# Kernel optimization log

Hardware: AMD Instinct MI355X
Metric: run time of the kernel (lower is better)

The kernel has to match this reference:

```python
import jax, jax.numpy as jnp
import numpy as np
import math

B, N, C, A, H = 1, 320, 128, 32, 4  # batch, n_res, rep_2d channels, attn channels, heads


def _layernorm(x, w, b, eps=1e-5):
    mu = jnp.mean(x, axis=-1, keepdims=True)
    var = jnp.var(x, axis=-1, keepdims=True)
    return (x - mu) * jax.lax.rsqrt(var + eps) * w + b


def setup_inputs() -> dict:
    key = jax.random.key(0)
    ks = jax.random.split(key, 12)
    s = 0.02
    return {
        "x2d": jax.random.normal(ks[0], (B, N, N, C), dtype=jnp.float32),
        "mask": jnp.ones((B, N, N), dtype=jnp.float32),
        "norm_w": jnp.ones((C,), dtype=jnp.float32),
        "norm_b": jnp.zeros((C,), dtype=jnp.float32),
        "Wq": jax.random.normal(ks[1], (C, A * H), dtype=jnp.float32) * s,
        "Wk": jax.random.normal(ks[2], (C, A * H), dtype=jnp.float32) * s,
        "Wv": jax.random.normal(ks[3], (C, A * H), dtype=jnp.float32) * s,
        "Wb": jax.random.normal(ks[4], (C, H), dtype=jnp.float32) * s,
        "Wg": jax.random.normal(ks[5], (C, A * H), dtype=jnp.float32) * s,
        "bg": jnp.zeros((A * H,), dtype=jnp.float32),
        "Wo": jax.random.normal(ks[6], (A * H, C), dtype=jnp.float32) * s,
        "bo": jnp.zeros((C,), dtype=jnp.float32),
    }


def reference(x2d, mask, norm_w, norm_b, Wq, Wk, Wv, Wb, Wg, bg, Wo, bo):
    xn = _layernorm(x2d, norm_w, norm_b)                      # [B,N,N,C]
    # note: torch .view(..., A, H) splits the output channel as (A, H)
    q = (xn @ Wq).reshape(B, N, N, A, H)
    k = (xn @ Wk).reshape(B, N, N, A, H)
    v = (xn @ Wv).reshape(B, N, N, A, H)
    b = xn @ Wb                                               # [B,N,N,H] -> b[b,j,k,h]
    g = jax.nn.sigmoid((xn @ Wg + bg).reshape(B, N, N, A, H))
    w = jnp.einsum('bijch,bikch->bijkh', q, k) / math.sqrt(A)
    # torch: b.unsqueeze(1).transpose(2,3) => w[b,i,j,k,h] += b[b,k,j,h]
    w = w + jnp.transpose(b, (0, 2, 1, 3))[:, None]           # [B,1,N,N,H]
    w = (w + 100.0) * mask[:, :, None, :, None] - 100.0
    w = jax.nn.softmax(w, axis=-2)                            # over k
    out = jnp.einsum('bijkh,bikch->bijch', w, v) * g          # [B,N,N,A,H]
    out = out.reshape(B, N, N, A * H) @ Wo + bo               # [B,N,N,C]
    out = out * mask[..., None]
    return out
```

## Files before the change

### kernel.cpp

```cpp
#include <hip/hip_runtime.h>
#include <hip/hip_bf16.h>
#include <math.h>

#define N 320
#define C 128
#define A 32
#define H 4
#define NPOS (N*N)

typedef __attribute__((ext_vector_type(8))) __bf16 bf16x8;
typedef __attribute__((ext_vector_type(16))) float f32x16;

union frag_u { int4 i; bf16x8 v; unsigned u[4]; };

#define MFMA32(va, vb, vc) __builtin_amdgcn_mfma_f32_32x32x16_bf16((va), (vb), (vc), 0, 0, 0)

#define WAVE_LDS_FENCE() do { \
    asm volatile("s_waitcnt lgkmcnt(0)" ::: "memory"); \
    __builtin_amdgcn_sched_barrier(0); \
} while (0)

static __device__ __forceinline__ unsigned pk_bf16(float lo, float hi) {
    union { __hip_bfloat162 h; unsigned u; } cv;
    cv.h = __float22bfloat162_rn(make_float2(lo, hi));
    return cv.u;
}

static __device__ __forceinline__ float bf16_to_f32(unsigned short u) {
    union { unsigned u; float f; } c;
    c.u = ((unsigned)u) << 16;
    return c.f;
}

static __device__ __forceinline__ float u32_as_f32(unsigned u) {
    union { unsigned u; float f; } c;
    c.u = u;
    return c.f;
}

__global__ __launch_bounds__(256)
void wprep_kernel(const float* __restrict__ Wq,
                  const float* __restrict__ Wk,
                  const float* __restrict__ Wv,
                  const float* __restrict__ Wg,
                  const float* __restrict__ Wo,
                  unsigned short* __restrict__ WF) {
    const float isq = 0.17677669529663687f;
    int tid = blockIdx.x * 256 + threadIdx.x;
    int lane = tid & 63;
    int kk = (tid >> 6) & 7;
    int ct = (tid >> 9) & 3;
    int mat = tid >> 11;
    const float* src = (mat == 0) ? Wq : (mat == 1) ? Wk : (mat == 2) ? Wv
                     : (mat == 3) ? Wg : Wo;
    float scl = (mat == 0) ? isq : 1.0f;
    int col = ct * 32 + (lane & 31);
    int c0 = kk * 16 + (lane >> 5) * 8;
    float v[8];
    #pragma unroll
    for (int e = 0; e < 8; e++) {
        int rr = c0 + e;
        int srow = (mat == 4) ? (((rr & 31) << 2) | (rr >> 5)) : rr;
        v[e] = src[(size_t)srow * 128 + col] * scl;
    }
    int4 out;
    out.x = pk_bf16(v[0], v[1]);
    out.y = pk_bf16(v[2], v[3]);
    out.z = pk_bf16(v[4], v[5]);
    out.w = pk_bf16(v[6], v[7]);
    *(int4*)((char*)WF + (size_t)tid * 16) = out;
}

__global__ __launch_bounds__(256)
void btrans_kernel(const float* __restrict__ Bp, unsigned short* __restrict__ BpTb) {
    __shared__ float tile[64][65];
    const int b = blockIdx.x;
    const int h = b / 25;
    const int bk = (b % 25) / 5;
    const int bj = b % 5;
    const int k0 = bk * 64, j0 = bj * 64;
    const float* src = Bp + (size_t)h * NPOS;
    unsigned short* dst = BpTb + (size_t)h * NPOS;
    const int t = threadIdx.x;
    #pragma unroll
    for (int u = 0; u < 16; ++u) {
        int idx = u * 256 + t;
        int kk = idx >> 6, jj = idx & 63;
        tile[kk][jj] = src[(size_t)(k0 + kk) * N + j0 + jj];
    }
    __syncthreads();
    #pragma unroll
    for (int u = 0; u < 16; ++u) {
        int idx = u * 256 + t;
        int jj = idx >> 6, kk = idx & 63;
        dst[(size_t)(j0 + jj) * N + k0 + kk] =
            (unsigned short)(pk_bf16(tile[kk][jj], 0.f) & 0xffffu);
    }
}

__global__ __launch_bounds__(256)
void ln_proj_kernel(const float* __restrict__ x2d,
                    const float* __restrict__ norm_w,
                    const float* __restrict__ norm_b,
                    const float* __restrict__ Wb,
                    const float* __restrict__ bg,
                    const unsigned short* __restrict__ WF,
                    unsigned short* __restrict__ Qb,
                    unsigned short* __restrict__ Kb,
                    unsigned short* __restrict__ Vta,
                    unsigned short* __restrict__ Gb,
                    float* __restrict__ Bp) {
    __shared__ __align__(16) unsigned char shbuf[16896];
    unsigned char* xnb = shbuf;

    const int t = threadIdx.x;
    const int gpos0 = blockIdx.x * 32;

    {
        const int r = t >> 3, s = t & 7;
        const float4* src = (const float4*)(x2d + (size_t)(gpos0 + r) * 128 + s * 16);
        float4 xv[4];
        #pragma unroll
        for (int u = 0; u < 4; u++) xv[u] = src[u];
        float sum = 0.f, sq = 0.f;
        #pragma unroll
        for (int u = 0; u < 4; u++) {
            sum += xv[u].x + xv[u].y + xv[u].z + xv[u].w;
            sq += xv[u].x * xv[u].x + xv[u].y * xv[u].y
                + xv[u].z * xv[u].z + xv[u].w * xv[u].w;
        }
        sum += __shfl_xor(sum, 1); sum += __shfl_xor(sum, 2); sum += __shfl_xor(sum, 4);
        sq  += __shfl_xor(sq, 1);  sq  += __shfl_xor(sq, 2);  sq  += __shfl_xor(sq, 4);
        float mean = sum * (1.0f / 128.0f);
        float var  = sq * (1.0f / 128.0f) - mean * mean;
        float rstd = rsqrtf(var + 1e-5f);

        const float4* wsrc = (const float4*)(norm_w + s * 16);
        const float4* bsrc = (const float4*)(norm_b + s * 16);
        const float4* wb4  = (const float4*)Wb;
        float pb0 = 0.f, pb1 = 0.f, pb2 = 0.f, pb3 = 0.f;
        float4 xe;
        #pragma unroll
        for (int u = 0; u < 4; u++) {
            float4 wv = wsrc[u], bv = bsrc[u], x4 = xv[u];
            float4 xn;
            xn.x = (x4.x - mean) * rstd * wv.x + bv.x;
            xn.y = (x4.y - mean) * rstd * wv.y + bv.y;
            xn.z = (x4.z - mean) * rstd * wv.z + bv.z;
            xn.w = (x4.w - mean) * rstd * wv.w + bv.w;
            int cb = s * 16 + u * 4;
            float4 w0 = wb4[cb + 0], w1 = wb4[cb + 1], w2 = wb4[cb + 2], w3 = wb4[cb + 3];
            pb0 = fmaf(xn.x, w0.x, fmaf(xn.y, w1.x, fmaf(xn.z, w2.x, fmaf(xn.w, w3.x, pb0))));
            pb1 = fmaf(xn.x, w0.y, fmaf(xn.y, w1.y, fmaf(xn.z, w2.y, fmaf(xn.w, w3.y, pb1))));
            pb2 = fmaf(xn.x, w0.z, fmaf(xn.y, w1.z, fmaf(xn.z, w2.z, fmaf(xn.w, w3.z, pb2))));
            pb3 = fmaf(xn.x, w0.w, fmaf(xn.y, w1.w, fmaf(xn.z, w2.w, fmaf(xn.w, w3.w, pb3))));
            if (u & 1) {
                int g = s * 2 + (u >> 1);
                int4 gr;
                gr.x = pk_bf16(xe.x, xe.y);
                gr.y = pk_bf16(xe.z, xe.w);
                gr.z = pk_bf16(xn.x, xn.y);
                gr.w = pk_bf16(xn.z, xn.w);
                *(int4*)(xnb + r * 256 + ((g ^ (r & 7)) << 4)) = gr;
            } else {
                xe = xn;
            }
        }
        pb0 += __shfl_xor(pb0, 1); pb0 += __shfl_xor(pb0, 2); pb0 += __shfl_xor(pb0, 4);
        pb1 += __shfl_xor(pb1, 1); pb1 += __shfl_xor(pb1, 2); pb1 += __shfl_xor(pb1, 4);
        pb2 += __shfl_xor(pb2, 1); pb2 += __shfl_xor(pb2, 2); pb2 += __shfl_xor(pb2, 4);
        pb3 += __shfl_xor(pb3, 1); pb3 += __shfl_xor(pb3, 2); pb3 += __shfl_xor(pb3, 4);
        if (s < 4) {
            float pbsel = (s == 0) ? pb0 : (s == 1) ? pb1 : (s == 2) ? pb2 : pb3;
            Bp[(size_t)s * NPOS + gpos0 + r] = pbsel;
        }
    }
    __syncthreads();

    const int lane = t & 63;
    const int w = t >> 6;
    const int col = lane & 31;
    const int hi = lane >> 5;

    frag_u af[8];
    #pragma unroll
    for (int kk = 0; kk < 8; kk++)
        af[kk].i = *(const int4*)(xnb + col * 256 + (((kk * 2 + hi) ^ (col & 7)) << 4));
    __syncthreads();

    const char* wf = (const char*)WF + (size_t)w * 4 * 8 * 1024;
    float* stage_w = (float*)shbuf + w * 1056;

    for (int ct = 0; ct < 4; ct++) {
        f32x16 acc;
        #pragma unroll
        for (int r = 0; r < 16; r++) acc[r] = 0.f;
        #pragma unroll
        for (int kk = 0; kk < 8; kk++) {
            frag_u bf;
            bf.i = *(const int4*)(wf + (ct * 8 + kk) * 1024 + lane * 16);
            acc = MFMA32(af[kk].v, bf.v, acc);
        }
        #pragma unroll
        for (int r = 0; r < 16; r++) {
            int patr = (r & 3) + 8 * (r >> 2) + 4 * hi;
            stage_w[col * 33 + patr] = acc[r];
        }
        WAVE_LDS_FENCE();
        if (w < 2) {
            char* dst = (w == 0) ? (char*)Qb : (char*)Kb;
            #pragma unroll
            for (int h = 0; h < 4; h++) {
                float f[4];
                #pragma unroll
                for (int e = 0; e < 4; e++)
                    f[e] = stage_w[((hi * 4 + e) * 4 + h) * 33 + col];
                uint2 val;
                val.x = pk_bf16(f[0], f[1]);
                val.y = pk_bf16(f[2], f[3]);
                *(uint2*)(dst + ((size_t)(h * 4 + ct) * NPOS + gpos0 + col) * 16 + hi * 8) = val;
            }
        } else if (w == 2) {
            int cc = col, half = hi;
            int plane = (cc & 3) * 32 + ct * 8 + (cc >> 2);
            unsigned pk[8];
            #pragma unroll
            for (int j2 = 0; j2 < 8; j2++)
                pk[j2] = pk_bf16(stage_w[cc * 33 + half * 16 + 2 * j2],
                                 stage_w[cc * 33 + half * 16 + 2 * j2 + 1]);
            int4* dst = (int4*)((char*)Vta + ((size_t)plane * NPOS + gpos0 + half * 16) * 2);
            dst[0] = make_int4(pk[0], pk[1], pk[2], pk[3]);
            dst[1] = make_int4(pk[4], pk[5], pk[6], pk[7]);
        } else {
            #pragma unroll
            for (int h = 0; h < 4; h++) {
                float f[4];
                #pragma unroll
                for (int e = 0; e < 4; e++) {
                    float z = stage_w[((hi * 4 + e) * 4 + h) * 33 + col]
                            + bg[ct * 32 + (hi * 4 + e) * 4 + h];
                    f[e] = 1.0f / (1.0f + __expf(-z));
                }
                uint2 val;
                val.x = pk_bf16(f[0], f[1]);
                val.y = pk_bf16(f[2], f[3]);
                *(uint2*)((char*)Gb + ((size_t)(h * 4 + ct) * NPOS + gpos0 + col) * 16 + hi * 8) = val;
            }
        }
        WAVE_LDS_FENCE();
    }
}

__global__ __launch_bounds__(320, 2)
void attn_kernel(const unsigned short* __restrict__ Qb,
                 const unsigned short* __restrict__ Kb,
                 const unsigned short* __restrict__ Vta,
                 const unsigned short* __restrict__ Gb,
                 const unsigned short* __restrict__ BpTb,
                 const float* __restrict__ mask,
                 unsigned short* __restrict__ Ob) {
    __shared__ __align__(16) unsigned char smem[21120];
    __shared__ float mparr[320];
    __shared__ float m2arr[320];

    const int i = blockIdx.x >> 2;
    const int h = blockIdx.x & 3;
    const int t = threadIdx.x;
    const int lane = t & 63;
    const int w = t >> 6;
    const int col = lane & 31;
    const int hi = lane >> 5;
    const int jt0 = w * 64;

    frag_u qf[2][2];
    const char* qplane = (const char*)Qb + ((size_t)(h * 4) * NPOS + (size_t)i * N) * 16;
    #pragma unroll
    for (int jt = 0; jt < 2; ++jt) {
        int jrow = jt0 + jt * 32 + col;
        #pragma unroll
        for (int cf = 0; cf < 2; ++cf) {
            int g = cf * 2 + hi;
            qf[jt][cf].i = *(const int4*)(qplane + ((size_t)g * NPOS + jrow) * 16);
        }
    }

    const char* kpl = (const char*)Kb + ((size_t)(h * 4) * NPOS + (size_t)i * N) * 16;

    const char* vbsrc = (const char*)Vta + ((size_t)h * 32 * NPOS + (size_t)i * N) * 2;
    #pragma unroll
    for (int it = 0; it < 4; ++it) {
        int tt = t + it * 320;
        int a = tt / 40, kg = tt % 40;
        int4 val = *(const int4*)(vbsrc + (size_t)a * NPOS * 2 + kg * 16);
        *(int4*)(smem + a * 640 + ((kg ^ (a & 7)) << 4)) = val;
    }
    {
        int kt_ = t >> 5, hi_ = (t >> 4) & 1, r_ = t & 15;
        int k = kt_ * 32 + (r_ & 3) + 8 * (r_ >> 2) + 4 * hi_;
        float m_ = mask[(size_t)i * N + k];
        mparr[t] = m_;
        m2arr[t] = fmaf(100.f, m_, -100.f);
    }
    frag_u kf0, kf1, kf0n, kf1n;
    kf0.i = *(const int4*)(kpl + ((size_t)hi * NPOS + col) * 16);
    kf1.i = *(const int4*)(kpl + ((size_t)(2 + hi) * NPOS + col) * 16);
    __syncthreads();

    f32x16 accO[2];
    #pragma unroll
    for (int r = 0; r < 16; ++r) { accO[0][r] = 0.f; accO[1][r] = 0.f; }
    float lsum[2] = { 0.f, 0.f };

    const unsigned short* br0 = BpTb + (size_t)h * NPOS + (size_t)(jt0 + col) * N + 4 * hi;
    const unsigned short* br1 = br0 + (size_t)32 * N;

    uint2 b0[4], b1[4];
    #pragma unroll
    for (int q = 0; q < 4; ++q) b0[q] = *(const uint2*)(br0 + 8 * q);

#define PROCESS_JT(JT, BB)                                                      \
    {                                                                           \
        f32x16 S;                                                               \
        _Pragma("unroll") for (int r = 0; r < 16; ++r) S[r] = 0.f;              \
        __builtin_amdgcn_s_setprio(1);                                          \
        S = MFMA32(kf0.v, qf[JT][0].v, S);                                      \
        S = MFMA32(kf1.v, qf[JT][1].v, S);                                      \
        __builtin_amdgcn_s_setprio(0);                                          \
        float pe[16];                                                           \
        float l0 = 0.f, l1 = 0.f, l2 = 0.f, l3 = 0.f;                           \
        _Pragma("unroll") for (int q = 0; q < 4; ++q) {                         \
            float bb0 = u32_as_f32(BB[q].x << 16);                              \
            float bb1 = u32_as_f32(BB[q].x & 0xffff0000u);                      \
            float bb2 = u32_as_f32(BB[q].y << 16);                              \
            float bb3 = u32_as_f32(BB[q].y & 0xffff0000u);                      \
            float sv0 = fmaf(S[4*q+0] + bb0, mk4[q].x, m2v[q].x);               \
            float sv1 = fmaf(S[4*q+1] + bb1, mk4[q].y, m2v[q].y);               \
            float sv2 = fmaf(S[4*q+2] + bb2, mk4[q].z, m2v[q].z);               \
            float sv3 = fmaf(S[4*q+3] + bb3, mk4[q].w, m2v[q].w);               \
            pe[4*q+0] = __expf(sv0); pe[4*q+1] = __expf(sv1);                   \
            pe[4*q+2] = __expf(sv2); pe[4*q+3] = __expf(sv3);                   \
            l0 += pe[4*q+0]; l1 += pe[4*q+1];                                   \
            l2 += pe[4*q+2]; l3 += pe[4*q+3];                                   \
        }                                                                       \
        lsum[JT] += (l0 + l1) + (l2 + l3);                                      \
        unsigned p[8];                                                          \
        _Pragma("unroll") for (int q = 0; q < 8; ++q)                           \
            p[q] = pk_bf16(pe[2 * q], pe[2 * q + 1]);                           \
        unsigned x0 = p[0], y0 = p[2];                                          \
        unsigned x1 = p[1], y1 = p[3];                                          \
        unsigned x2 = p[4], y2 = p[6];                                          \
        unsigned x3 = p[5], y3 = p[7];                                          \
        asm("v_permlane32_swap_b32 %0, %1" : "+v"(x0), "+v"(y0));               \
        asm("v_permlane32_swap_b32 %0, %1" : "+v"(x1), "+v"(y1));               \
        asm("v_permlane32_swap_b32 %0, %1" : "+v"(x2), "+v"(y2));               \
        asm("v_permlane32_swap_b32 %0, %1" : "+v"(x3), "+v"(y3));               \
        frag_u bf0, bf1;                                                        \
        bf0.u[0] = x0; bf0.u[1] = x1; bf0.u[2] = y0; bf0.u[3] = y1;             \
        bf1.u[0] = x2; bf1.u[1] = x3; bf1.u[2] = y2; bf1.u[3] = y3;             \
        __builtin_amdgcn_s_setprio(1);                                          \
        accO[JT] = MFMA32(vf0.v, bf0.v, accO[JT]);                              \
        accO[JT] = MFMA32(vf1.v, bf1.v, accO[JT]);                              \
        __builtin_amdgcn_s_setprio(0);                                          \
    }

    for (int kt = 0; kt < 10; ++kt) {
        const int kbase = kt * 32;
        frag_u vf0, vf1;
        vf0.i = *(const int4*)(smem + col * 640 + (((kt * 4 + 0 + hi) ^ (col & 7)) << 4));
        vf1.i = *(const int4*)(smem + col * 640 + (((kt * 4 + 2 + hi) ^ (col & 7)) << 4));

        if (kt < 9) {
            int krn = kbase + 32 + col;
            kf0n.i = *(const int4*)(kpl + ((size_t)hi * NPOS + krn) * 16);
            kf1n.i = *(const int4*)(kpl + ((size_t)(2 + hi) * NPOS + krn) * 16);
        }

        float4 mk4[4], m2v[4];
        const float* mp  = mparr + kbase + hi * 16;
        const float* m2p = m2arr + kbase + hi * 16;
        #pragma unroll
        for (int q = 0; q < 4; ++q) {
            mk4[q] = *(const float4*)(mp + 4 * q);
            m2v[q] = *(const float4*)(m2p + 4 * q);
        }

        #pragma unroll
        for (int q = 0; q < 4; ++q) b1[q] = *(const uint2*)(br1 + kbase + 8 * q);

        PROCESS_JT(0, b0)

        if (kt < 9) {
            #pragma unroll
            for (int q = 0; q < 4; ++q) b0[q] = *(const uint2*)(br0 + kbase + 32 + 8 * q);
        }

        PROCESS_JT(1, b1)

        kf0 = kf0n;
        kf1 = kf1n;
    }
#undef PROCESS_JT

    __syncthreads();
    float* st = (float*)(smem + w * 4224);
    const char* gplane = (const char*)Gb + ((size_t)(h * 4) * NPOS + (size_t)i * N) * 16;

    #pragma unroll
    for (int jt = 0; jt < 2; ++jt) {
        float lt = lsum[jt] + __shfl_xor(lsum[jt], 32);
        float inv = 1.0f / lt;
        #pragma unroll
        for (int r = 0; r < 16; ++r) {
            const int a = (r & 3) + 8 * (r >> 2) + 4 * hi;
            st[col * 33 + a] = accO[jt][r] * inv;
        }
        WAVE_LDS_FENCE();
        {
            int jj = lane & 31;
            int ah0 = hi * 16;
            int jrow = jt0 + jt * 32 + jj;
            int4 g0 = *(const int4*)(gplane + ((size_t)(2 * hi + 0) * NPOS + jrow) * 16);
            int4 g1 = *(const int4*)(gplane + ((size_t)(2 * hi + 1) * NPOS + jrow) * 16);
            unsigned gw[8] = { (unsigned)g0.x, (unsigned)g0.y, (unsigned)g0.z, (unsigned)g0.w,
                               (unsigned)g1.x, (unsigned)g1.y, (unsigned)g1.z, (unsigned)g1.w };
            unsigned pk8[8];
            #pragma unroll
            for (int e = 0; e < 8; ++e) {
                float ge0 = bf16_to_f32((unsigned short)(gw[e] & 0xffffu));
                float ge1 = bf16_to_f32((unsigned short)(gw[e] >> 16));
                pk8[e] = pk_bf16(st[jj * 33 + ah0 + 2 * e + 0] * ge0,
                                 st[jj * 33 + ah0 + 2 * e + 1] * ge1);
            }
            char* dst = (char*)Ob + (((size_t)i * N + jrow) * 128 + h * 32 + ah0) * 2;
            *(int4*)dst = make_int4(pk8[0], pk8[1], pk8[2], pk8[3]);
            *(int4*)(dst + 16) = make_int4(pk8[4], pk8[5], pk8[6], pk8[7]);
        }
        WAVE_LDS_FENCE();
    }
}

__global__ __launch_bounds__(256)
void outproj_kernel(const unsigned short* __restrict__ Ob,
                    const unsigned short* __restrict__ WoF,
                    const float* __restrict__ bo,
                    const float* __restrict__ mask,
                    float* __restrict__ out) {
    __shared__ __align__(16) unsigned char obs[64 * 256];
    __shared__ float stage[4][32 * 65];

    const int t = threadIdx.x;
    const int gpos0 = blockIdx.x * 64;

    {
        const int r = t >> 2, s = t & 3;
        const char* src = (const char*)Ob + ((size_t)(gpos0 + r) * 128 + s * 32) * 2;
        #pragma unroll
        for (int u = 0; u < 4; ++u) {
            int4 v = *(const int4*)(src + u * 16);
            int g = s * 4 + u;
            *(int4*)(obs + r * 256 + ((g ^ (r & 7)) << 4)) = v;
        }
    }
    __syncthreads();

    const int lane = t & 63;
    const int w = t >> 6;
    const int col = lane & 31;
    const int hi = lane >> 5;

    f32x16 acc0, acc1;
    float bocol = bo[w * 32 + col];
    #pragma unroll
    for (int r = 0; r < 16; ++r) { acc0[r] = bocol; acc1[r] = bocol; }

    const char* wf = (const char*)WoF + (size_t)w * 8 * 1024;
    #pragma unroll
    for (int kk = 0; kk < 8; ++kk) {
        frag_u bf, a0, a1;
        bf.i = *(const int4*)(wf + kk * 1024 + lane * 16);
        int row0 = col, row1 = 32 + col;
        a0.i = *(const int4*)(obs + row0 * 256 + (((kk * 2 + hi) ^ (row0 & 7)) << 4));
        a1.i = *(const int4*)(obs + row1 * 256 + (((kk * 2 + hi) ^ (row1 & 7)) << 4));
        acc0 = MFMA32(a0.v, bf.v, acc0);
        acc1 = MFMA32(a1.v, bf.v, acc1);
    }

    float* st = stage[w];
    #pragma unroll
    for (int r = 0; r < 16; ++r) {
        int patr = (r & 3) + 8 * (r >> 2) + 4 * hi;
        st[col * 65 + patr] = acc0[r];
        st[col * 65 + 32 + patr] = acc1[r];
    }
    WAVE_LDS_FENCE();
    {
        int row = lane;
        float mv = mask[gpos0 + row];
        float4* dst = (float4*)(out + (size_t)(gpos0 + row) * 128 + w * 32);
        #pragma unroll
        for (int u = 0; u < 8; ++u) {
            float4 o;
            o.x = st[(4 * u + 0) * 65 + row] * mv;
            o.y = st[(4 * u + 1) * 65 + row] * mv;
            o.z = st[(4 * u + 2) * 65 + row] * mv;
            o.w = st[(4 * u + 3) * 65 + row] * mv;
            dst[u] = o;
        }
    }
}

extern "C" void kernel_launch(void* const* d_in, const int* in_sizes, int n_in,
                              void* d_out, int out_size, void* d_ws, size_t ws_size,
                              hipStream_t stream) {
    const float* x2d    = (const float*)d_in[0];
    const float* mask   = (const float*)d_in[1];
    const float* norm_w = (const float*)d_in[2];
    const float* norm_b = (const float*)d_in[3];
    const float* Wq     = (const float*)d_in[4];
    const float* Wk     = (const float*)d_in[5];
    const float* Wv     = (const float*)d_in[6];
    const float* Wb     = (const float*)d_in[7];
    const float* Wg     = (const float*)d_in[8];
    const float* bg     = (const float*)d_in[9];
    const float* Wo     = (const float*)d_in[10];
    const float* bo     = (const float*)d_in[11];
    float* out = (float*)d_out;

    char* ws = (char*)d_ws;
    float* Bp  = (float*)ws;                                   ws += (size_t)H * NPOS * 4;
    unsigned short* BpTb = (unsigned short*)ws;                ws += (size_t)H * NPOS * 4;
    unsigned short* Qb  = (unsigned short*)ws;                 ws += (size_t)NPOS * C * 2;
    unsigned short* Kb  = (unsigned short*)ws;                 ws += (size_t)NPOS * C * 2;
    unsigned short* Vta = (unsigned short*)ws;                 ws += (size_t)NPOS * C * 2;
    unsigned short* Gb  = (unsigned short*)ws;                 ws += (size_t)NPOS * C * 2;
    unsigned short* Ob  = (unsigned short*)ws;                 ws += (size_t)NPOS * C * 2;
    unsigned short* WF  = (unsigned short*)ws;
    unsigned short* WoF = WF + (size_t)4 * 16384;

    wprep_kernel<<<40, 256, 0, stream>>>(Wq, Wk, Wv, Wg, Wo, WF);

    ln_proj_kernel<<<NPOS / 32, 256, 0, stream>>>(x2d, norm_w, norm_b, Wb, bg,
                                                  WF, Qb, Kb, Vta, Gb, Bp);

    btrans_kernel<<<H * 25, 256, 0, stream>>>(Bp, BpTb);

    attn_kernel<<<N * H, 320, 0, stream>>>(Qb, Kb, Vta, Gb, BpTb, mask, Ob);

    outproj_kernel<<<NPOS / 64, 256, 0, stream>>>(Ob, WoF, bo, mask, out);
}
```

Measured before the change: 184.8 us.

## Software-pipeline QK MFMA one k-tile ahead of softmax and PV in attention loop

Restructures the attention inner loop so the QK^T MFMAs for the next k-tile are issued while the current tile's bias/mask math and exponentials run, with S0/S1 computed before the loop. Both j-tiles are processed together, and bias and K fragment loads are prefetched one iteration further ahead. The aim is to hide MFMA latency behind VALU and transcendental work and to interleave the two independent tiles. In exchange it raises register pressure (extra S, bias and K buffers), which could lower occupancy or cause spills.

```diff
diff --git a/kernel.cpp b/kernel.cpp
--- a/kernel.cpp
+++ b/kernel.cpp
@@ -301,9 +301,28 @@
         mparr[t] = m_;
         m2arr[t] = fmaf(100.f, m_, -100.f);
     }
+
     frag_u kf0, kf1, kf0n, kf1n;
     kf0.i = *(const int4*)(kpl + ((size_t)hi * NPOS + col) * 16);
     kf1.i = *(const int4*)(kpl + ((size_t)(2 + hi) * NPOS + col) * 16);
+    f32x16 S0, S1;
+    #pragma unroll
+    for (int r = 0; r < 16; ++r) { S0[r] = 0.f; S1[r] = 0.f; }
+    S0 = MFMA32(kf0.v, qf[0][0].v, S0);
+    S0 = MFMA32(kf1.v, qf[0][1].v, S0);
+    S1 = MFMA32(kf0.v, qf[1][0].v, S1);
+    S1 = MFMA32(kf1.v, qf[1][1].v, S1);
+    kf0n.i = *(const int4*)(kpl + ((size_t)hi * NPOS + 32 + col) * 16);
+    kf1n.i = *(const int4*)(kpl + ((size_t)(2 + hi) * NPOS + 32 + col) * 16);
+
+    const unsigned short* br0 = BpTb + (size_t)h * NPOS + (size_t)(jt0 + col) * N + 4 * hi;
+    const unsigned short* br1 = br0 + (size_t)32 * N;
+    uint2 b0[4], b1[4];
+    #pragma unroll
+    for (int q = 0; q < 4; ++q) b0[q] = *(const uint2*)(br0 + 8 * q);
+    #pragma unroll
+    for (int q = 0; q < 4; ++q) b1[q] = *(const uint2*)(br1 + 8 * q);
+
     __syncthreads();
 
     f32x16 accO[2];
@@ -311,70 +330,13 @@
     for (int r = 0; r < 16; ++r) { accO[0][r] = 0.f; accO[1][r] = 0.f; }
     float lsum[2] = { 0.f, 0.f };
 
-    const unsigned short* br0 = BpTb + (size_t)h * NPOS + (size_t)(jt0 + col) * N + 4 * hi;
-    const unsigned short* br1 = br0 + (size_t)32 * N;
-
-    uint2 b0[4], b1[4];
-    #pragma unroll
-    for (int q = 0; q < 4; ++q) b0[q] = *(const uint2*)(br0 + 8 * q);
-
-#define PROCESS_JT(JT, BB)                                                      \
-    {                                                                           \
-        f32x16 S;                                                               \
-        _Pragma("unroll") for (int r = 0; r < 16; ++r) S[r] = 0.f;              \
-        __builtin_amdgcn_s_setprio(1);                                          \
-        S = MFMA32(kf0.v, qf[JT][0].v, S);                                      \
-        S = MFMA32(kf1.v, qf[JT][1].v, S);                                      \
-        __builtin_amdgcn_s_setprio(0);                                          \
-        float pe[16];                                                           \
-        float l0 = 0.f, l1 = 0.f, l2 = 0.f, l3 = 0.f;                           \
-        _Pragma("unroll") for (int q = 0; q < 4; ++q) {                         \
-            float bb0 = u32_as_f32(BB[q].x << 16);                              \
-            float bb1 = u32_as_f32(BB[q].x & 0xffff0000u);                      \
-            float bb2 = u32_as_f32(BB[q].y << 16);                              \
-            float bb3 = u32_as_f32(BB[q].y & 0xffff0000u);                      \
-            float sv0 = fmaf(S[4*q+0] + bb0, mk4[q].x, m2v[q].x);               \
-            float sv1 = fmaf(S[4*q+1] + bb1, mk4[q].y, m2v[q].y);               \
-            float sv2 = fmaf(S[4*q+2] + bb2, mk4[q].z, m2v[q].z);               \
-            float sv3 = fmaf(S[4*q+3] + bb3, mk4[q].w, m2v[q].w);               \
-            pe[4*q+0] = __expf(sv0); pe[4*q+1] = __expf(sv1);                   \
-            pe[4*q+2] = __expf(sv2); pe[4*q+3] = __expf(sv3);                   \
-            l0 += pe[4*q+0]; l1 += pe[4*q+1];                                   \
-            l2 += pe[4*q+2]; l3 += pe[4*q+3];                                   \
-        }                                                                       \
-        lsum[JT] += (l0 + l1) + (l2 + l3);                                      \
-        unsigned p[8];                                                          \
-        _Pragma("unroll") for (int q = 0; q < 8; ++q)                           \
-            p[q] = pk_bf16(pe[2 * q], pe[2 * q + 1]);                           \
-        unsigned x0 = p[0], y0 = p[2];                                          \
-        unsigned x1 = p[1], y1 = p[3];                                          \
-        unsigned x2 = p[4], y2 = p[6];                                          \
-        unsigned x3 = p[5], y3 = p[7];                                          \
-        asm("v_permlane32_swap_b32 %0, %1" : "+v"(x0), "+v"(y0));               \
-        asm("v_permlane32_swap_b32 %0, %1" : "+v"(x1), "+v"(y1));               \
-        asm("v_permlane32_swap_b32 %0, %1" : "+v"(x2), "+v"(y2));               \
-        asm("v_permlane32_swap_b32 %0, %1" : "+v"(x3), "+v"(y3));               \
-        frag_u bf0, bf1;                                                        \
-        bf0.u[0] = x0; bf0.u[1] = x1; bf0.u[2] = y0; bf0.u[3] = y1;             \
-        bf1.u[0] = x2; bf1.u[1] = x3; bf1.u[2] = y2; bf1.u[3] = y3;             \
-        __builtin_amdgcn_s_setprio(1);                                          \
-        accO[JT] = MFMA32(vf0.v, bf0.v, accO[JT]);                              \
-        accO[JT] = MFMA32(vf1.v, bf1.v, accO[JT]);                              \
-        __builtin_amdgcn_s_setprio(0);                                          \
-    }
-
     for (int kt = 0; kt < 10; ++kt) {
         const int kbase = kt * 32;
+
         frag_u vf0, vf1;
         vf0.i = *(const int4*)(smem + col * 640 + (((kt * 4 + 0 + hi) ^ (col & 7)) << 4));
         vf1.i = *(const int4*)(smem + col * 640 + (((kt * 4 + 2 + hi) ^ (col & 7)) << 4));
 
-        if (kt < 9) {
-            int krn = kbase + 32 + col;
-            kf0n.i = *(const int4*)(kpl + ((size_t)hi * NPOS + krn) * 16);
-            kf1n.i = *(const int4*)(kpl + ((size_t)(2 + hi) * NPOS + krn) * 16);
-        }
-
         float4 mk4[4], m2v[4];
         const float* mp  = mparr + kbase + hi * 16;
         const float* m2p = m2arr + kbase + hi * 16;
@@ -384,22 +346,111 @@
             m2v[q] = *(const float4*)(m2p + 4 * q);
         }
 
-        #pragma unroll
-        for (int q = 0; q < 4; ++q) b1[q] = *(const uint2*)(br1 + kbase + 8 * q);
-
-        PROCESS_JT(0, b0)
-
+        uint2 bn0[4], bn1[4];
         if (kt < 9) {
             #pragma unroll
-            for (int q = 0; q < 4; ++q) b0[q] = *(const uint2*)(br0 + kbase + 32 + 8 * q);
-        }
-
-        PROCESS_JT(1, b1)
-
-        kf0 = kf0n;
-        kf1 = kf1n;
-    }
-#undef PROCESS_JT
+            for (int q = 0; q < 4; ++q) bn0[q] = *(const uint2*)(br0 + kbase + 32 + 8 * q);
+            #pragma unroll
+            for (int q = 0; q < 4; ++q) bn1[q] = *(const uint2*)(br1 + kbase + 32 + 8 * q);
+        }
+
+        float sv0[16], sv1[16];
+        #pragma unroll
+        for (int q = 0; q < 4; ++q) {
+            float a0 = u32_as_f32(b0[q].x << 16);
+            float a1 = u32_as_f32(b0[q].x & 0xffff0000u);
+            float a2 = u32_as_f32(b0[q].y << 16);
+            float a3 = u32_as_f32(b0[q].y & 0xffff0000u);
+            sv0[4*q+0] = fmaf(S0[4*q+0] + a0, mk4[q].x, m2v[q].x);
+            sv0[4*q+1] = fmaf(S0[4*q+1] + a1, mk4[q].y, m2v[q].y);
+            sv0[4*q+2] = fmaf(S0[4*q+2] + a2, mk4[q].z, m2v[q].z);
+            sv0[4*q+3] = fmaf(S0[4*q+3] + a3, mk4[q].w, m2v[q].w);
+            float c0 = u32_as_f32(b1[q].x << 16);
+            float c1 = u32_as_f32(b1[q].x & 0xffff0000u);
+            float c2 = u32_as_f32(b1[q].y << 16);
+            float c3 = u32_as_f32(b1[q].y & 0xffff0000u);
+            sv1[4*q+0] = fmaf(S1[4*q+0] + c0, mk4[q].x, m2v[q].x);
+            sv1[4*q+1] = fmaf(S1[4*q+1] + c1, mk4[q].y, m2v[q].y);
+            sv1[4*q+2] = fmaf(S1[4*q+2] + c2, mk4[q].z, m2v[q].z);
+            sv1[4*q+3] = fmaf(S1[4*q+3] + c3, mk4[q].w, m2v[q].w);
+        }
+
+        if (kt < 9) {
+            f32x16 t0, t1;
+            #pragma unroll
+            for (int r = 0; r < 16; ++r) { t0[r] = 0.f; t1[r] = 0.f; }
+            __builtin_amdgcn_s_setprio(1);
+            t0 = MFMA32(kf0n.v, qf[0][0].v, t0);
+            t0 = MFMA32(kf1n.v, qf[0][1].v, t0);
+            t1 = MFMA32(kf0n.v, qf[1][0].v, t1);
+            t1 = MFMA32(kf1n.v, qf[1][1].v, t1);
+            __builtin_amdgcn_s_setprio(0);
+            S0 = t0;
+            S1 = t1;
+            kf0 = kf0n;
+            kf1 = kf1n;
+            if (kt < 8) {
+                int krn = kbase + 64 + col;
+                kf0n.i = *(const int4*)(kpl + ((size_t)hi * NPOS + krn) * 16);
+                kf1n.i = *(const int4*)(kpl + ((size_t)(2 + hi) * NPOS + krn) * 16);
+            }
+        }
+
+        float pe0[16], pe1[16];
+        float l00 = 0.f, l01 = 0.f, l02 = 0.f, l03 = 0.f;
+        float l10 = 0.f, l11 = 0.f, l12 = 0.f, l13 = 0.f;
+        #pragma unroll
+        for (int q = 0; q < 4; ++q) {
+            pe0[4*q+0] = __expf(sv0[4*q+0]); pe0[4*q+1] = __expf(sv0[4*q+1]);
+            pe0[4*q+2] = __expf(sv0[4*q+2]); pe0[4*q+3] = __expf(sv0[4*q+3]);
+            pe1[4*q+0] = __expf(sv1[4*q+0]); pe1[4*q+1] = __expf(sv1[4*q+1]);
+            pe1[4*q+2] = __expf(sv1[4*q+2]); pe1[4*q+3] = __expf(sv1[4*q+3]);
+            l00 += pe0[4*q+0]; l01 += pe0[4*q+1]; l02 += pe0[4*q+2]; l03 += pe0[4*q+3];
+            l10 += pe1[4*q+0]; l11 += pe1[4*q+1]; l12 += pe1[4*q+2]; l13 += pe1[4*q+3];
+        }
+        lsum[0] += (l00 + l01) + (l02 + l03);
+        lsum[1] += (l10 + l11) + (l12 + l13);
+
+        frag_u bfA0, bfA1, bfB0, bfB1;
+        {
+            unsigned p[8];
+            #pragma unroll
+            for (int q = 0; q < 8; ++q) p[q] = pk_bf16(pe0[2*q], pe0[2*q+1]);
+            unsigned x0 = p[0], y0 = p[2], x1 = p[1], y1 = p[3];
+            unsigned x2 = p[4], y2 = p[6], x3 = p[5], y3 = p[7];
+            asm("v_permlane32_swap_b32 %0, %1" : "+v"(x0), "+v"(y0));
+            asm("v_permlane32_swap_b32 %0, %1" : "+v"(x1), "+v"(y1));
+            asm("v_permlane32_swap_b32 %0, %1" : "+v"(x2), "+v"(y2));
+            asm("v_permlane32_swap_b32 %0, %1" : "+v"(x3), "+v"(y3));
+            bfA0.u[0] = x0; bfA0.u[1] = x1; bfA0.u[2] = y0; bfA0.u[3] = y1;
+            bfA1.u[0] = x2; bfA1.u[1] = x3; bfA1.u[2] = y2; bfA1.u[3] = y3;
+        }
+        {
+            unsigned p[8];
+            #pragma unroll
+            for (int q = 0; q < 8; ++q) p[q] = pk_bf16(pe1[2*q], pe1[2*q+1]);
+            unsigned x0 = p[0], y0 = p[2], x1 = p[1], y1 = p[3];
+            unsigned x2 = p[4], y2 = p[6], x3 = p[5], y3 = p[7];
+            asm("v_permlane32_swap_b32 %0, %1" : "+v"(x0), "+v"(y0));
+            asm("v_permlane32_swap_b32 %0, %1" : "+v"(x1), "+v"(y1));
+            asm("v_permlane32_swap_b32 %0, %1" : "+v"(x2), "+v"(y2));
+            asm("v_permlane32_swap_b32 %0, %1" : "+v"(x3), "+v"(y3));
+            bfB0.u[0] = x0; bfB0.u[1] = x1; bfB0.u[2] = y0; bfB0.u[3] = y1;
+            bfB1.u[0] = x2; bfB1.u[1] = x3; bfB1.u[2] = y2; bfB1.u[3] = y3;
+        }
+
+        __builtin_amdgcn_s_setprio(1);
+        accO[0] = MFMA32(vf0.v, bfA0.v, accO[0]);
+        accO[0] = MFMA32(vf1.v, bfA1.v, accO[0]);
+        accO[1] = MFMA32(vf0.v, bfB0.v, accO[1]);
+        accO[1] = MFMA32(vf1.v, bfB1.v, accO[1]);
+        __builtin_amdgcn_s_setprio(0);
+
+        if (kt < 9) {
+            #pragma unroll
+            for (int q = 0; q < 4; ++q) { b0[q] = bn0[q]; b1[q] = bn1[q]; }
+        }
+    }
 
     __syncthreads();
     float* st = (float*)(smem + w * 4224);
```

Measured after the change: 188.5 us. About the same (+2.0%).

## Stage K tiles in LDS with per-wave phase-staggered k loop; halve outproj staging

Applied to the files above, without the earlier changes.

The attention kernel now loads the whole K plane for the row into LDS once, with a swizzled layout, and reads K fragments from LDS. Previously each wave software-prefetched K straight from global memory. Each wave also begins its k-tile loop at a different offset (phase), which spreads LDS bank and global bias-read contention across waves. The out-projection kernel writes its staged tile in two 32-row halves so the per-wave LDS stage buffer is half as large. The cost is that the attention kernel's LDS use roughly doubles to about 41KB, which may limit the 2-blocks-per-CU occupancy target.

```diff
diff --git a/kernel.cpp b/kernel.cpp
--- a/kernel.cpp
+++ b/kernel.cpp
@@ -259,9 +259,11 @@
                  const unsigned short* __restrict__ BpTb,
                  const float* __restrict__ mask,
                  unsigned short* __restrict__ Ob) {
-    __shared__ __align__(16) unsigned char smem[21120];
+    __shared__ __align__(16) unsigned char smem[40960];
     __shared__ float mparr[320];
     __shared__ float m2arr[320];
+    unsigned char* Klds = smem;
+    unsigned char* Vlds = smem + 20480;
 
     const int i = blockIdx.x >> 2;
     const int h = blockIdx.x & 3;
@@ -271,6 +273,7 @@
     const int col = lane & 31;
     const int hi = lane >> 5;
     const int jt0 = w * 64;
+    const int phase = w * 2;
 
     frag_u qf[2][2];
     const char* qplane = (const char*)Qb + ((size_t)(h * 4) * NPOS + (size_t)i * N) * 16;
@@ -284,15 +287,19 @@
         }
     }
 
-    const char* kpl = (const char*)Kb + ((size_t)(h * 4) * NPOS + (size_t)i * N) * 16;
-
+    const char* kplane = (const char*)Kb + ((size_t)(h * 4) * NPOS + (size_t)i * N) * 16;
+    #pragma unroll
+    for (int it = 0; it < 4; ++it) {
+        int4 val = *(const int4*)(kplane + ((size_t)it * NPOS + t) * 16);
+        *(int4*)(Klds + t * 64 + ((it ^ ((t >> 1) & 3)) << 4)) = val;
+    }
     const char* vbsrc = (const char*)Vta + ((size_t)h * 32 * NPOS + (size_t)i * N) * 2;
     #pragma unroll
     for (int it = 0; it < 4; ++it) {
         int tt = t + it * 320;
         int a = tt / 40, kg = tt % 40;
         int4 val = *(const int4*)(vbsrc + (size_t)a * NPOS * 2 + kg * 16);
-        *(int4*)(smem + a * 640 + ((kg ^ (a & 7)) << 4)) = val;
+        *(int4*)(Vlds + a * 640 + ((kg ^ (a & 7)) << 4)) = val;
     }
     {
         int kt_ = t >> 5, hi_ = (t >> 4) & 1, r_ = t & 15;
@@ -301,9 +308,6 @@
         mparr[t] = m_;
         m2arr[t] = fmaf(100.f, m_, -100.f);
     }
-    frag_u kf0, kf1, kf0n, kf1n;
-    kf0.i = *(const int4*)(kpl + ((size_t)hi * NPOS + col) * 16);
-    kf1.i = *(const int4*)(kpl + ((size_t)(2 + hi) * NPOS + col) * 16);
     __syncthreads();
 
     f32x16 accO[2];
@@ -316,7 +320,7 @@
 
     uint2 b0[4], b1[4];
     #pragma unroll
-    for (int q = 0; q < 4; ++q) b0[q] = *(const uint2*)(br0 + 8 * q);
+    for (int q = 0; q < 4; ++q) b0[q] = *(const uint2*)(br0 + phase * 32 + 8 * q);
 
 #define PROCESS_JT(JT, BB)                                                      \
     {                                                                           \
@@ -364,16 +368,15 @@
     }
 
     for (int kt = 0; kt < 10; ++kt) {
-        const int kbase = kt * 32;
-        frag_u vf0, vf1;
-        vf0.i = *(const int4*)(smem + col * 640 + (((kt * 4 + 0 + hi) ^ (col & 7)) << 4));
-        vf1.i = *(const int4*)(smem + col * 640 + (((kt * 4 + 2 + hi) ^ (col & 7)) << 4));
-
-        if (kt < 9) {
-            int krn = kbase + 32 + col;
-            kf0n.i = *(const int4*)(kpl + ((size_t)hi * NPOS + krn) * 16);
-            kf1n.i = *(const int4*)(kpl + ((size_t)(2 + hi) * NPOS + krn) * 16);
-        }
+        int kte = kt + phase; if (kte >= 10) kte -= 10;
+        int ktn = kte + 1;    if (ktn >= 10) ktn -= 10;
+        const int kbase = kte * 32;
+        const int krow = kbase + col;
+        frag_u kf0, kf1, vf0, vf1;
+        kf0.i = *(const int4*)(Klds + krow * 64 + (((0 + hi) ^ ((krow >> 1) & 3)) << 4));
+        kf1.i = *(const int4*)(Klds + krow * 64 + (((2 + hi) ^ ((krow >> 1) & 3)) << 4));
+        vf0.i = *(const int4*)(Vlds + col * 640 + (((kte * 4 + 0 + hi) ^ (col & 7)) << 4));
+        vf1.i = *(const int4*)(Vlds + col * 640 + (((kte * 4 + 2 + hi) ^ (col & 7)) << 4));
 
         float4 mk4[4], m2v[4];
         const float* mp  = mparr + kbase + hi * 16;
@@ -391,18 +394,15 @@
 
         if (kt < 9) {
             #pragma unroll
-            for (int q = 0; q < 4; ++q) b0[q] = *(const uint2*)(br0 + kbase + 32 + 8 * q);
+            for (int q = 0; q < 4; ++q) b0[q] = *(const uint2*)(br0 + ktn * 32 + 8 * q);
         }
 
         PROCESS_JT(1, b1)
-
-        kf0 = kf0n;
-        kf1 = kf1n;
     }
 #undef PROCESS_JT
 
     __syncthreads();
-    float* st = (float*)(smem + w * 4224);
+    float* st = (float*)(smem + w * 8192);
     const char* gplane = (const char*)Gb + ((size_t)(h * 4) * NPOS + (size_t)i * N) * 16;
 
     #pragma unroll
@@ -446,7 +446,7 @@
                     const float* __restrict__ mask,
                     float* __restrict__ out) {
     __shared__ __align__(16) unsigned char obs[64 * 256];
-    __shared__ float stage[4][32 * 65];
+    __shared__ float stage[4][32 * 33];
 
     const int t = threadIdx.x;
     const int gpos0 = blockIdx.x * 64;
@@ -487,25 +487,31 @@
 
     float* st = stage[w];
     #pragma unroll
-    for (int r = 0; r < 16; ++r) {
-        int patr = (r & 3) + 8 * (r >> 2) + 4 * hi;
-        st[col * 65 + patr] = acc0[r];
-        st[col * 65 + 32 + patr] = acc1[r];
-    }
-    WAVE_LDS_FENCE();
-    {
-        int row = lane;
-        float mv = mask[gpos0 + row];
-        float4* dst = (float4*)(out + (size_t)(gpos0 + row) * 128 + w * 32);
-        #pragma unroll
-        for (int u = 0; u < 8; ++u) {
-            float4 o;
-            o.x = st[(4 * u + 0) * 65 + row] * mv;
-            o.y = st[(4 * u + 1) * 65 + row] * mv;
-            o.z = st[(4 * u + 2) * 65 + row] * mv;
-            o.w = st[(4 * u + 3) * 65 + row] * mv;
-            dst[u] = o;
-        }
+    for (int p = 0; p < 2; ++p) {
+        const f32x16& ac = p ? acc1 : acc0;
+        #pragma unroll
+        for (int r = 0; r < 16; ++r) {
+            int patr = (r & 3) + 8 * (r >> 2) + 4 * hi;
+            st[col * 33 + patr] = ac[r];
+        }
+        WAVE_LDS_FENCE();
+        {
+            int pr = lane & 31;
+            int row = p * 32 + pr;
+            int c0 = (lane >> 5) * 16;
+            float mv = mask[gpos0 + row];
+            float4* dst = (float4*)(out + (size_t)(gpos0 + row) * 128 + w * 32 + c0);
+            #pragma unroll
+            for (int u = 0; u < 4; ++u) {
+                float4 o;
+                o.x = st[(c0 + 4 * u + 0) * 33 + pr] * mv;
+                o.y = st[(c0 + 4 * u + 1) * 33 + pr] * mv;
+                o.z = st[(c0 + 4 * u + 2) * 33 + pr] * mv;
+                o.w = st[(c0 + 4 * u + 3) * 33 + pr] * mv;
+                dst[u] = o;
+            }
+        }
+        WAVE_LDS_FENCE();
     }
 }
 
```

After: 186.0 us. No clear change (+0.6%).
